# Optimization experiments

Hardware: AMD Instinct MI355X
Metric: run time of the kernel (lower is better)

## Reference

```python
import jax, jax.numpy as jnp
import numpy as np

N_EXPERTS, D_MODEL, D_FF, TOP_K, N_TOKENS = 8, 1024, 4096, 2, 8192

def _uniform_init(key, shape, fan_in):
    # matches torch init: gain = sqrt(1/3), std = gain/sqrt(fan_in), bound = sqrt(3)*std
    bound = np.sqrt(3.0) * np.sqrt(1.0 / 3.0) / np.sqrt(fan_in)
    return jax.random.uniform(key, shape, minval=-bound, maxval=bound, dtype=jnp.float32)

def setup_inputs() -> dict:
    key = jax.random.key(0)
    kx, ki, kw, k1, k2, k3 = jax.random.split(key, 6)
    x = jax.random.normal(kx, (N_TOKENS, D_MODEL), dtype=jnp.float32)
    expert_indices = jax.random.randint(ki, (N_TOKENS, TOP_K), 0, N_EXPERTS, dtype=jnp.int32)
    expert_weights = jax.random.uniform(kw, (N_TOKENS, TOP_K), dtype=jnp.float32)
    w1 = _uniform_init(k1, (N_EXPERTS, D_MODEL, D_FF), D_MODEL)
    w2 = _uniform_init(k2, (N_EXPERTS, D_MODEL, D_FF), D_MODEL)
    w3 = _uniform_init(k3, (N_EXPERTS, D_FF, D_MODEL), D_FF)
    return {"x": x, "expert_indices": expert_indices, "expert_weights": expert_weights,
            "w1": w1, "w2": w2, "w3": w3}

def reference(x, expert_indices, expert_weights, w1, w2, w3):
    # For each token t and routed expert e with routing weight p:
    #   out[t] += p * (silu(x[t] @ W1[e]) * (x[t] @ W2[e])) @ W3[e]
    # Loop over the small fixed expert set; compute each expert's SwiGLU FFN
    # densely over all tokens and combine with per-token routing weights
    # (mathematically identical to the sorted-dispatch grouped GEMM).
    n_experts = w1.shape[0]
    out = jnp.zeros_like(x)
    for e in range(n_experts):
        gate = x @ w1[e]                 # [N, d_ff]
        val = x @ w2[e]                  # [N, d_ff]
        y = (jax.nn.silu(gate) * val) @ w3[e]   # [N, d_model]
        # sum routing weights over top_k slots that picked expert e
        p = jnp.sum(jnp.where(expert_indices == e, expert_weights, 0.0), axis=1)
        out = out + p[:, None] * y
    return out
```

## Files before the change

kernel.cpp:

```cpp
#include <hip/hip_runtime.h>
#include <hip/hip_bf16.h>

typedef __attribute__((ext_vector_type(8))) short short8;
typedef __attribute__((ext_vector_type(4))) float f32x4;
typedef unsigned short u16;
typedef unsigned int u32;

#define NTOK   8192
#define DMODEL 1024
#define DFF    4096
#define NEXP   8
#define NPAIR  (NTOK * 2)
#define PADM   256
#define MT1    72
#define PPAD   (MT1 * PADM)
#define MT2    (PPAD / 128)

#define OFF_XB   0ull
#define OFF_W1T  (OFF_XB  + (size_t)NTOK * DMODEL * 2)
#define OFF_W2T  (OFF_W1T + (size_t)NEXP * DFF * DMODEL * 2)
#define OFF_W3T  (OFF_W2T + (size_t)NEXP * DFF * DMODEL * 2)
#define OFF_H    (OFF_W3T + (size_t)NEXP * DMODEL * DFF * 2)
#define OFF_TOK  (OFF_H   + (size_t)PPAD * DFF * 2)
#define OFF_WGT  (OFF_TOK + (size_t)PPAD * 4)
#define OFF_CNT  (OFF_WGT + (size_t)PPAD * 4)
#define OFF_CUR  (OFF_CNT + 64)
#define OFF_OFFP (OFF_CUR + 64)
#define WS_END   (OFF_OFFP + 64)

#define GLOAD16(gp, lp)                                                        \
  __builtin_amdgcn_global_load_lds(                                            \
      (const __attribute__((address_space(1))) u32*)(gp),                      \
      (__attribute__((address_space(3))) u32*)(lp), 16, 0, 0)

__device__ __forceinline__ u16 f2bu(float f) {
  __hip_bfloat16 b = __float2bfloat16(f);
  return __builtin_bit_cast(u16, b);
}


__global__ __launch_bounds__(256) void cvt_x_k(const float* __restrict__ x,
                                               u16* __restrict__ xb) {
  int i = blockIdx.x * 256 + threadIdx.x;
  float4 v = ((const float4*)x)[i];
  unsigned long long pk = (unsigned long long)f2bu(v.x) |
                          ((unsigned long long)f2bu(v.y) << 16) |
                          ((unsigned long long)f2bu(v.z) << 32) |
                          ((unsigned long long)f2bu(v.w) << 48);
  ((unsigned long long*)xb)[i] = pk;
}

__global__ __launch_bounds__(256) void tr_cvt_k(const float* __restrict__ src,
                                                u16* __restrict__ dst, int R, int C) {
  src += (size_t)blockIdx.z * R * C;
  dst += (size_t)blockIdx.z * R * C;
  int c0 = blockIdx.x * 64, r0 = blockIdx.y * 64;
  __shared__ float tile[64][65];
  int tid = threadIdx.x;
  int f4 = tid & 15, rr = tid >> 4;
#pragma unroll
  for (int p = 0; p < 4; ++p) {
    int r = rr + p * 16;
    float4 v = *(const float4*)(src + (size_t)(r0 + r) * C + c0 + f4 * 4);
    tile[r][f4 * 4 + 0] = v.x; tile[r][f4 * 4 + 1] = v.y;
    tile[r][f4 * 4 + 2] = v.z; tile[r][f4 * 4 + 3] = v.w;
  }
  __syncthreads();
  int ch = tid & 7, cc = tid >> 3;
#pragma unroll
  for (int p = 0; p < 2; ++p) {
    int c = cc + p * 32;
    short8 s;
#pragma unroll
    for (int j = 0; j < 8; ++j) s[j] = (short)f2bu(tile[ch * 8 + j][c]);
    *(short8*)(dst + (size_t)(c0 + c) * R + r0 + ch * 8) = s;
  }
}


__global__ __launch_bounds__(256) void count_k(const int* __restrict__ ei,
                                               int* __restrict__ cnt) {
  int i = blockIdx.x * 256 + threadIdx.x;
  atomicAdd(&cnt[ei[i]], 1);
}

__global__ void scan_k(const int* __restrict__ cnt, int* __restrict__ offp) {
  if (threadIdx.x == 0) {
    int a = 0;
#pragma unroll
    for (int e = 0; e < NEXP; ++e) { offp[e] = a; a += (cnt[e] + PADM - 1) & ~(PADM - 1); }
    offp[NEXP] = a;
  }
}

__global__ __launch_bounds__(256) void scatter_k(const int* __restrict__ ei,
                                                 const float* __restrict__ ew,
                                                 const int* __restrict__ offp,
                                                 int* __restrict__ cur,
                                                 int* __restrict__ tok,
                                                 float* __restrict__ wg) {
  int i = blockIdx.x * 256 + threadIdx.x;
  int e = ei[i];
  int p = offp[e] + atomicAdd(&cur[e], 1);
  tok[p] = i >> 1;
  wg[p] = ew[i];
}


#define S1_BUF 16384
#define S1_NK  32

__global__ __launch_bounds__(512, 2) void stage1_k(const u16* __restrict__ xb,
                                                   const u16* __restrict__ w1t,
                                                   const u16* __restrict__ w2t,
                                                   u16* __restrict__ h,
                                                   const int* __restrict__ tok,
                                                   const int* __restrict__ offp) {
  extern __shared__ __align__(16) u16 lds[];
  const int r0 = blockIdx.y * PADM;
  if (r0 >= offp[NEXP]) return;
  int e = 0;
#pragma unroll
  for (int q = 0; q < 7; ++q) e += (offp[e + 1] <= r0) ? 1 : 0;
  const int n0 = blockIdx.x * 128;
  const int tid = threadIdx.x;
  const int lane = tid & 63, w = tid >> 6;
  const int wm = w >> 2, wn = w & 3;

  const int sl = lane & 3, rl = lane >> 2;
  const u16* aga[2];
  int adb[2];
#pragma unroll
  for (int j = 0; j < 2; ++j) {
    int row = w * 32 + j * 16 + rl;
    int t = tok[r0 + row];
    aga[j] = xb + (size_t)t * DMODEL + ((sl ^ ((row >> 1) & 3)) << 3);
    adb[j] = (w * 32 + j * 16) * 32;
  }
  const u16* w1e = w1t + (size_t)e * DFF * DMODEL;
  const u16* w2e = w2t + (size_t)e * DFF * DMODEL;
  const u16* bg1; const u16* bg2;
  int bdb;
  {
    int row = w * 16 + rl;
    size_t ro = (size_t)(n0 + row) * DMODEL + ((sl ^ ((row >> 1) & 3)) << 3);
    bg1 = w1e + ro; bg2 = w2e + ro;
    bdb = (w * 16) * 32;
  }

  int aoff[8], boff[2];
  {
    int ks = lane >> 4;
#pragma unroll
    for (int mi = 0; mi < 8; ++mi) {
      int row = wm * 128 + mi * 16 + (lane & 15);
      aoff[mi] = row * 32 + ((ks ^ ((row >> 1) & 3)) << 3);
    }
#pragma unroll
    for (int ni = 0; ni < 2; ++ni) {
      int col = wn * 32 + ni * 16 + (lane & 15);
      boff[ni] = col * 32 + ((ks ^ ((col >> 1) & 3)) << 3);
    }
  }

  f32x4 accg[8][2], accv[8][2];
  const f32x4 zero = {0.f, 0.f, 0.f, 0.f};
#pragma unroll
  for (int mi = 0; mi < 8; ++mi)
#pragma unroll
    for (int ni = 0; ni < 2; ++ni) { accg[mi][ni] = zero; accv[mi][ni] = zero; }

#define S1_ISSUE(Q, KO)                                                        \
  do {                                                                         \
    GLOAD16(aga[0] + (KO), (Q) + adb[0]);                                      \
    GLOAD16(aga[1] + (KO), (Q) + adb[1]);                                      \
    GLOAD16(bg1 + (KO), (Q) + 8192 + bdb);                                     \
    GLOAD16(bg2 + (KO), (Q) + 12288 + bdb);                                    \
  } while (0)

  S1_ISSUE(lds, 0);
  S1_ISSUE(lds + S1_BUF, 32);
  asm volatile("s_waitcnt vmcnt(4)" ::: "memory");
  __builtin_amdgcn_s_barrier();
  __builtin_amdgcn_sched_barrier(0);

#define S1_STEP(P, KC, ISSUE)                                                  \
  {                                                                            \
    const u16* Ab  = lds + (P) * S1_BUF;                                       \
    const u16* B1b = Ab + 8192;                                                \
    const u16* B2b = Ab + 12288;                                               \
    short8 af[8], b1f[2], b2f[2];                                              \
    _Pragma("unroll") for (int mi = 0; mi < 8; ++mi)                           \
      af[mi] = *(const short8*)(Ab + aoff[mi]);                                \
    _Pragma("unroll") for (int ni = 0; ni < 2; ++ni) {                         \
      b1f[ni] = *(const short8*)(B1b + boff[ni]);                              \
      b2f[ni] = *(const short8*)(B2b + boff[ni]);                              \
    }                                                                          \
    if (ISSUE) S1_ISSUE(lds + (((P) + 2) % 3) * S1_BUF, ((KC) + 2) * 32);      \
    __builtin_amdgcn_s_setprio(1);                                             \
    _Pragma("unroll") for (int mi = 0; mi < 8; ++mi)                           \
      _Pragma("unroll") for (int ni = 0; ni < 2; ++ni) {                       \
        accg[mi][ni] = __builtin_amdgcn_mfma_f32_16x16x32_bf16(                \
            af[mi], b1f[ni], accg[mi][ni], 0, 0, 0);                           \
        accv[mi][ni] = __builtin_amdgcn_mfma_f32_16x16x32_bf16(                \
            af[mi], b2f[ni], accv[mi][ni], 0, 0, 0);                           \
      }                                                                        \
    __builtin_amdgcn_s_setprio(0);                                             \
    if (ISSUE) asm volatile("s_waitcnt vmcnt(4)" ::: "memory");                \
    else       asm volatile("s_waitcnt vmcnt(0)" ::: "memory");                \
    __builtin_amdgcn_s_barrier();                                              \
    __builtin_amdgcn_sched_barrier(0);                                         \
  }

  for (int kc = 0; kc < S1_NK - 2; kc += 3) {
    S1_STEP(0, kc, 1)
    S1_STEP(1, kc + 1, 1)
    S1_STEP(2, kc + 2, 1)
  }
  S1_STEP(0, S1_NK - 2, 0)
  S1_STEP(1, S1_NK - 1, 0)
#undef S1_STEP
#undef S1_ISSUE

  const int prow = r0 + wm * 128 + ((lane >> 4) << 2);
  const int pcol = n0 + wn * 32 + (lane & 15);
#pragma unroll
  for (int mi = 0; mi < 8; ++mi)
#pragma unroll
    for (int ni = 0; ni < 2; ++ni)
#pragma unroll
      for (int j = 0; j < 4; ++j) {
        float g = accg[mi][ni][j];
        float v = accv[mi][ni][j];
        float s = g / (1.f + __expf(-g));
        h[(size_t)(prow + mi * 16 + j) * DFF + (pcol + ni * 16)] = f2bu(s * v);
      }
}


__global__ __launch_bounds__(256) void stage2_k(const u16* __restrict__ h,
                                                const u16* __restrict__ w3t,
                                                float* __restrict__ out,
                                                const int* __restrict__ tok,
                                                const float* __restrict__ wg,
                                                const int* __restrict__ offp) {
  __shared__ __align__(16) u16 As[128 * 64];
  __shared__ __align__(16) u16 Bs[64 * 64];
  const int r0 = blockIdx.y * 128;
  if (r0 >= offp[NEXP]) return;
  int e = 0;
#pragma unroll
  for (int q = 0; q < 7; ++q) e += (offp[e + 1] <= r0) ? 1 : 0;
  const int n0 = blockIdx.x * 64;
  const int tid = threadIdx.x;
  const int lane = tid & 63, w = tid >> 6;
  const int wm = w >> 1, wn = w & 1;
  const int lr = lane >> 3, seg = lane & 7;

  const u16* aga[4];
#pragma unroll
  for (int j = 0; j < 4; ++j) {
    int rowl = w * 32 + j * 8 + lr;
    aga[j] = h + (size_t)(r0 + rowl) * DFF + ((seg ^ (rowl & 7)) << 3);
  }
  const u16* w3e = w3t + (size_t)e * DMODEL * DFF;
  const u16* bga[2];
#pragma unroll
  for (int j = 0; j < 2; ++j) {
    int coll = w * 16 + j * 8 + lr;
    bga[j] = w3e + (size_t)(n0 + coll) * DFF + ((seg ^ (coll & 7)) << 3);
  }
  u16 *Ad[4], *Bd[2];
#pragma unroll
  for (int j = 0; j < 4; ++j) Ad[j] = As + (w * 32 + j * 8) * 64;
#pragma unroll
  for (int j = 0; j < 2; ++j) Bd[j] = Bs + (w * 16 + j * 8) * 64;

  int aoff[4][2], boff[2][2];
  {
    int ar = wm * 64 + (lane & 15), ks = lane >> 4;
#pragma unroll
    for (int mi = 0; mi < 4; ++mi)
#pragma unroll
      for (int kk = 0; kk < 2; ++kk) {
        int row = ar + mi * 16;
        aoff[mi][kk] = row * 64 + (((kk * 4 + ks) ^ (row & 7)) << 3);
      }
    int bc = wn * 32 + (lane & 15);
#pragma unroll
    for (int ni = 0; ni < 2; ++ni)
#pragma unroll
      for (int kk = 0; kk < 2; ++kk) {
        int col = bc + ni * 16;
        boff[ni][kk] = col * 64 + (((kk * 4 + ks) ^ (col & 7)) << 3);
      }
  }

  f32x4 acc[4][2];
  const f32x4 zero = {0.f, 0.f, 0.f, 0.f};
#pragma unroll
  for (int mi = 0; mi < 4; ++mi)
#pragma unroll
    for (int ni = 0; ni < 2; ++ni) acc[mi][ni] = zero;

  for (int kc = 0; kc < DFF / 64; ++kc) {
    const int ko = kc * 64;
#pragma unroll
    for (int j = 0; j < 4; ++j) GLOAD16(aga[j] + ko, Ad[j]);
#pragma unroll
    for (int j = 0; j < 2; ++j) GLOAD16(bga[j] + ko, Bd[j]);
    __syncthreads();
#pragma unroll
    for (int kk = 0; kk < 2; ++kk) {
      short8 a[4], b[2];
#pragma unroll
      for (int mi = 0; mi < 4; ++mi) a[mi] = *(const short8*)(As + aoff[mi][kk]);
#pragma unroll
      for (int ni = 0; ni < 2; ++ni) b[ni] = *(const short8*)(Bs + boff[ni][kk]);
#pragma unroll
      for (int mi = 0; mi < 4; ++mi)
#pragma unroll
        for (int ni = 0; ni < 2; ++ni)
          acc[mi][ni] = __builtin_amdgcn_mfma_f32_16x16x32_bf16(a[mi], b[ni], acc[mi][ni], 0, 0, 0);
    }
    __syncthreads();
  }

  const int prow = r0 + wm * 64 + ((lane >> 4) << 2);
  const int pcol = n0 + wn * 32 + (lane & 15);
#pragma unroll
  for (int mi = 0; mi < 4; ++mi)
#pragma unroll
    for (int j = 0; j < 4; ++j) {
      int pos = prow + mi * 16 + j;
      float p = wg[pos];
      if (p != 0.f) {
        int t = tok[pos];
#pragma unroll
        for (int ni = 0; ni < 2; ++ni)
          atomicAdd(&out[(size_t)t * DMODEL + pcol + ni * 16], p * acc[mi][ni][j]);
      }
    }
}


extern "C" void kernel_launch(void* const* d_in, const int* in_sizes, int n_in,
                              void* d_out, int out_size, void* d_ws, size_t ws_size,
                              hipStream_t stream) {
  (void)in_sizes; (void)n_in;
  const float* x  = (const float*)d_in[0];
  const int*   ei = (const int*)d_in[1];
  const float* ew = (const float*)d_in[2];
  const float* w1 = (const float*)d_in[3];
  const float* w2 = (const float*)d_in[4];
  const float* w3 = (const float*)d_in[5];
  float* out = (float*)d_out;
  char* ws = (char*)d_ws;

  hipMemsetAsync(out, 0, (size_t)out_size * sizeof(float), stream);
  if (ws_size < WS_END) return;

  u16* xb   = (u16*)(ws + OFF_XB);
  u16* w1t  = (u16*)(ws + OFF_W1T);
  u16* w2t  = (u16*)(ws + OFF_W2T);
  u16* w3t  = (u16*)(ws + OFF_W3T);
  u16* hb   = (u16*)(ws + OFF_H);
  int* tok  = (int*)(ws + OFF_TOK);
  float* wg = (float*)(ws + OFF_WGT);
  int* cnt  = (int*)(ws + OFF_CNT);
  int* cur  = (int*)(ws + OFF_CUR);
  int* offp = (int*)(ws + OFF_OFFP);

  hipMemsetAsync(ws + OFF_TOK, 0, (size_t)(WS_END - OFF_TOK), stream);

  hipFuncSetAttribute(reinterpret_cast<const void*>(stage1_k),
                      hipFuncAttributeMaxDynamicSharedMemorySize, 98304);

  cvt_x_k<<<dim3(NTOK * DMODEL / 4 / 256), 256, 0, stream>>>(x, xb);
  tr_cvt_k<<<dim3(DFF / 64, DMODEL / 64, NEXP), 256, 0, stream>>>(w1, w1t, DMODEL, DFF);
  tr_cvt_k<<<dim3(DFF / 64, DMODEL / 64, NEXP), 256, 0, stream>>>(w2, w2t, DMODEL, DFF);
  tr_cvt_k<<<dim3(DMODEL / 64, DFF / 64, NEXP), 256, 0, stream>>>(w3, w3t, DFF, DMODEL);
  count_k<<<dim3(NPAIR / 256), 256, 0, stream>>>(ei, cnt);
  scan_k<<<1, 64, 0, stream>>>(cnt, offp);
  scatter_k<<<dim3(NPAIR / 256), 256, 0, stream>>>(ei, ew, offp, cur, tok, wg);
  stage1_k<<<dim3(DFF / 128, MT1), 512, 98304, stream>>>(xb, w1t, w2t, hb, tok, offp);
  stage2_k<<<dim3(DMODEL / 64, MT2), 256, 0, stream>>>(hb, w3t, out, tok, wg, offp);
}
```

Baseline: 842.5 us.

## Use 32x32 MFMA in stage1 and pipeline stage2 with larger tiles

Stage1 switches from 16x16x32 to 32x32x16 bf16 MFMA instructions, cutting the number of LDS fragment reads per MFMA and changing the epilogue row mapping. Stage2 is rewritten from a single-buffered 128x64 tile with 256 threads to a 256x128 tile with 512 threads and a triple-buffered global_load_lds pipeline in dynamic LDS, modelled on stage1. This aims to overlap W3/h loads with compute and raise data reuse in the down-projection. The cost is higher register and LDS use per block, fewer blocks, and more atomics per thread in the epilogue.

```diff
diff --git a/kernel.cpp b/kernel.cpp
--- a/kernel.cpp
+++ b/kernel.cpp
@@ -3,6 +3,7 @@
 
 typedef __attribute__((ext_vector_type(8))) short short8;
 typedef __attribute__((ext_vector_type(4))) float f32x4;
+typedef __attribute__((ext_vector_type(16))) float f32x16;
 typedef unsigned short u16;
 typedef unsigned int u32;
 
@@ -14,7 +15,6 @@
 #define PADM   256
 #define MT1    72
 #define PPAD   (MT1 * PADM)
-#define MT2    (PPAD / 128)
 
 #define OFF_XB   0ull
 #define OFF_W1T  (OFF_XB  + (size_t)NTOK * DMODEL * 2)
@@ -148,27 +148,24 @@
     bdb = (w * 16) * 32;
   }
 
-  int aoff[8], boff[2];
+  int aoff[4], boff;
   {
-    int ks = lane >> 4;
-#pragma unroll
-    for (int mi = 0; mi < 8; ++mi) {
-      int row = wm * 128 + mi * 16 + (lane & 15);
-      aoff[mi] = row * 32 + ((ks ^ ((row >> 1) & 3)) << 3);
+    int kg0 = lane >> 5;
+#pragma unroll
+    for (int mb = 0; mb < 4; ++mb) {
+      int row = wm * 128 + mb * 32 + (lane & 31);
+      aoff[mb] = row * 32 + ((kg0 ^ ((row >> 1) & 3)) << 3);
     }
-#pragma unroll
-    for (int ni = 0; ni < 2; ++ni) {
-      int col = wn * 32 + ni * 16 + (lane & 15);
-      boff[ni] = col * 32 + ((ks ^ ((col >> 1) & 3)) << 3);
-    }
-  }
-
-  f32x4 accg[8][2], accv[8][2];
-  const f32x4 zero = {0.f, 0.f, 0.f, 0.f};
-#pragma unroll
-  for (int mi = 0; mi < 8; ++mi)
-#pragma unroll
-    for (int ni = 0; ni < 2; ++ni) { accg[mi][ni] = zero; accv[mi][ni] = zero; }
+    int col = wn * 32 + (lane & 31);
+    boff = col * 32 + ((kg0 ^ ((col >> 1) & 3)) << 3);
+  }
+
+  f32x16 accg[4], accv[4];
+#pragma unroll
+  for (int mb = 0; mb < 4; ++mb) {
+#pragma unroll
+    for (int r = 0; r < 16; ++r) { accg[mb][r] = 0.f; accv[mb][r] = 0.f; }
+  }
 
 #define S1_ISSUE(Q, KO)                                                        \
   do {                                                                         \
@@ -189,21 +186,22 @@
     const u16* Ab  = lds + (P) * S1_BUF;                                       \
     const u16* B1b = Ab + 8192;                                                \
     const u16* B2b = Ab + 12288;                                               \
-    short8 af[8], b1f[2], b2f[2];                                              \
-    _Pragma("unroll") for (int mi = 0; mi < 8; ++mi)                           \
-      af[mi] = *(const short8*)(Ab + aoff[mi]);                                \
-    _Pragma("unroll") for (int ni = 0; ni < 2; ++ni) {                         \
-      b1f[ni] = *(const short8*)(B1b + boff[ni]);                              \
-      b2f[ni] = *(const short8*)(B2b + boff[ni]);                              \
+    short8 af[4][2], b1f[2], b2f[2];                                           \
+    _Pragma("unroll") for (int mb = 0; mb < 4; ++mb)                           \
+      _Pragma("unroll") for (int kk = 0; kk < 2; ++kk)                         \
+        af[mb][kk] = *(const short8*)(Ab + (aoff[mb] ^ (kk << 4)));            \
+    _Pragma("unroll") for (int kk = 0; kk < 2; ++kk) {                         \
+      b1f[kk] = *(const short8*)(B1b + (boff ^ (kk << 4)));                    \
+      b2f[kk] = *(const short8*)(B2b + (boff ^ (kk << 4)));                    \
     }                                                                          \
     if (ISSUE) S1_ISSUE(lds + (((P) + 2) % 3) * S1_BUF, ((KC) + 2) * 32);      \
     __builtin_amdgcn_s_setprio(1);                                             \
-    _Pragma("unroll") for (int mi = 0; mi < 8; ++mi)                           \
-      _Pragma("unroll") for (int ni = 0; ni < 2; ++ni) {                       \
-        accg[mi][ni] = __builtin_amdgcn_mfma_f32_16x16x32_bf16(                \
-            af[mi], b1f[ni], accg[mi][ni], 0, 0, 0);                           \
-        accv[mi][ni] = __builtin_amdgcn_mfma_f32_16x16x32_bf16(                \
-            af[mi], b2f[ni], accv[mi][ni], 0, 0, 0);                           \
+    _Pragma("unroll") for (int kk = 0; kk < 2; ++kk)                           \
+      _Pragma("unroll") for (int mb = 0; mb < 4; ++mb) {                       \
+        accg[mb] = __builtin_amdgcn_mfma_f32_32x32x16_bf16(                    \
+            af[mb][kk], b1f[kk], accg[mb], 0, 0, 0);                           \
+        accv[mb] = __builtin_amdgcn_mfma_f32_32x32x16_bf16(                    \
+            af[mb][kk], b2f[kk], accv[mb], 0, 0, 0);                           \
       }                                                                        \
     __builtin_amdgcn_s_setprio(0);                                             \
     if (ISSUE) asm volatile("s_waitcnt vmcnt(4)" ::: "memory");                \
@@ -222,112 +220,140 @@
 #undef S1_STEP
 #undef S1_ISSUE
 
-  const int prow = r0 + wm * 128 + ((lane >> 4) << 2);
-  const int pcol = n0 + wn * 32 + (lane & 15);
-#pragma unroll
-  for (int mi = 0; mi < 8; ++mi)
-#pragma unroll
-    for (int ni = 0; ni < 2; ++ni)
-#pragma unroll
-      for (int j = 0; j < 4; ++j) {
-        float g = accg[mi][ni][j];
-        float v = accv[mi][ni][j];
-        float s = g / (1.f + __expf(-g));
-        h[(size_t)(prow + mi * 16 + j) * DFF + (pcol + ni * 16)] = f2bu(s * v);
-      }
-}
-
-
-__global__ __launch_bounds__(256) void stage2_k(const u16* __restrict__ h,
-                                                const u16* __restrict__ w3t,
-                                                float* __restrict__ out,
-                                                const int* __restrict__ tok,
-                                                const float* __restrict__ wg,
-                                                const int* __restrict__ offp) {
-  __shared__ __align__(16) u16 As[128 * 64];
-  __shared__ __align__(16) u16 Bs[64 * 64];
-  const int r0 = blockIdx.y * 128;
+  const int ecol = n0 + wn * 32 + (lane & 31);
+  const int erow0 = r0 + wm * 128 + 4 * (lane >> 5);
+#pragma unroll
+  for (int mb = 0; mb < 4; ++mb)
+#pragma unroll
+    for (int r = 0; r < 16; ++r) {
+      int erow = erow0 + mb * 32 + (r & 3) + 8 * (r >> 2);
+      float g = accg[mb][r];
+      float v = accv[mb][r];
+      float s = g / (1.f + __expf(-g));
+      h[(size_t)erow * DFF + ecol] = f2bu(s * v);
+    }
+}
+
+
+#define S2_BUF 12288
+#define S2_NK  128
+
+__global__ __launch_bounds__(512, 4) void stage2_k(const u16* __restrict__ h,
+                                                   const u16* __restrict__ w3t,
+                                                   float* __restrict__ out,
+                                                   const int* __restrict__ tok,
+                                                   const float* __restrict__ wg,
+                                                   const int* __restrict__ offp) {
+  extern __shared__ __align__(16) u16 lds[];
+  const int r0 = blockIdx.y * 256;
   if (r0 >= offp[NEXP]) return;
   int e = 0;
 #pragma unroll
   for (int q = 0; q < 7; ++q) e += (offp[e + 1] <= r0) ? 1 : 0;
-  const int n0 = blockIdx.x * 64;
+  const int n0 = blockIdx.x * 128;
   const int tid = threadIdx.x;
   const int lane = tid & 63, w = tid >> 6;
   const int wm = w >> 1, wn = w & 1;
-  const int lr = lane >> 3, seg = lane & 7;
-
-  const u16* aga[4];
-#pragma unroll
-  for (int j = 0; j < 4; ++j) {
-    int rowl = w * 32 + j * 8 + lr;
-    aga[j] = h + (size_t)(r0 + rowl) * DFF + ((seg ^ (rowl & 7)) << 3);
+
+  const int sl = lane & 3, rl = lane >> 2;
+  const u16* aga[2];
+  int adb[2];
+#pragma unroll
+  for (int j = 0; j < 2; ++j) {
+    int row = w * 32 + j * 16 + rl;
+    aga[j] = h + (size_t)(r0 + row) * DFF + ((sl ^ ((row >> 1) & 3)) << 3);
+    adb[j] = (w * 32 + j * 16) * 32;
   }
   const u16* w3e = w3t + (size_t)e * DMODEL * DFF;
-  const u16* bga[2];
-#pragma unroll
-  for (int j = 0; j < 2; ++j) {
-    int coll = w * 16 + j * 8 + lr;
-    bga[j] = w3e + (size_t)(n0 + coll) * DFF + ((seg ^ (coll & 7)) << 3);
-  }
-  u16 *Ad[4], *Bd[2];
-#pragma unroll
-  for (int j = 0; j < 4; ++j) Ad[j] = As + (w * 32 + j * 8) * 64;
-#pragma unroll
-  for (int j = 0; j < 2; ++j) Bd[j] = Bs + (w * 16 + j * 8) * 64;
-
-  int aoff[4][2], boff[2][2];
+  const u16* bga;
+  int bdb;
   {
-    int ar = wm * 64 + (lane & 15), ks = lane >> 4;
-#pragma unroll
-    for (int mi = 0; mi < 4; ++mi)
-#pragma unroll
-      for (int kk = 0; kk < 2; ++kk) {
-        int row = ar + mi * 16;
-        aoff[mi][kk] = row * 64 + (((kk * 4 + ks) ^ (row & 7)) << 3);
-      }
-    int bc = wn * 32 + (lane & 15);
-#pragma unroll
-    for (int ni = 0; ni < 2; ++ni)
-#pragma unroll
-      for (int kk = 0; kk < 2; ++kk) {
-        int col = bc + ni * 16;
-        boff[ni][kk] = col * 64 + (((kk * 4 + ks) ^ (col & 7)) << 3);
-      }
-  }
-
-  f32x4 acc[4][2];
+    int row = w * 16 + rl;
+    bga = w3e + (size_t)(n0 + row) * DFF + ((sl ^ ((row >> 1) & 3)) << 3);
+    bdb = (w * 16) * 32;
+  }
+
+  int aoff[4], boff[4];
+  {
+    int ks = lane >> 4;
+#pragma unroll
+    for (int mi = 0; mi < 4; ++mi) {
+      int row = wm * 64 + mi * 16 + (lane & 15);
+      aoff[mi] = row * 32 + ((ks ^ ((row >> 1) & 3)) << 3);
+    }
+#pragma unroll
+    for (int ni = 0; ni < 4; ++ni) {
+      int col = wn * 64 + ni * 16 + (lane & 15);
+      boff[ni] = col * 32 + ((ks ^ ((col >> 1) & 3)) << 3);
+    }
+  }
+
+  f32x4 acc[4][4];
   const f32x4 zero = {0.f, 0.f, 0.f, 0.f};
 #pragma unroll
   for (int mi = 0; mi < 4; ++mi)
 #pragma unroll
-    for (int ni = 0; ni < 2; ++ni) acc[mi][ni] = zero;
-
-  for (int kc = 0; kc < DFF / 64; ++kc) {
-    const int ko = kc * 64;
-#pragma unroll
-    for (int j = 0; j < 4; ++j) GLOAD16(aga[j] + ko, Ad[j]);
-#pragma unroll
-    for (int j = 0; j < 2; ++j) GLOAD16(bga[j] + ko, Bd[j]);
-    __syncthreads();
-#pragma unroll
-    for (int kk = 0; kk < 2; ++kk) {
-      short8 a[4], b[2];
-#pragma unroll
-      for (int mi = 0; mi < 4; ++mi) a[mi] = *(const short8*)(As + aoff[mi][kk]);
-#pragma unroll
-      for (int ni = 0; ni < 2; ++ni) b[ni] = *(const short8*)(Bs + boff[ni][kk]);
-#pragma unroll
-      for (int mi = 0; mi < 4; ++mi)
-#pragma unroll
-        for (int ni = 0; ni < 2; ++ni)
-          acc[mi][ni] = __builtin_amdgcn_mfma_f32_16x16x32_bf16(a[mi], b[ni], acc[mi][ni], 0, 0, 0);
-    }
-    __syncthreads();
-  }
+    for (int ni = 0; ni < 4; ++ni) acc[mi][ni] = zero;
+
+#define S2_ISSUE(Q, KO)                                                        \
+  do {                                                                         \
+    GLOAD16(aga[0] + (KO), (Q) + adb[0]);                                      \
+    GLOAD16(aga[1] + (KO), (Q) + adb[1]);                                      \
+    GLOAD16(bga + (KO), (Q) + 8192 + bdb);                                     \
+  } while (0)
+
+  S2_ISSUE(lds, 0);
+  S2_ISSUE(lds + S2_BUF, 32);
+  asm volatile("s_waitcnt vmcnt(3)" ::: "memory");
+  __builtin_amdgcn_s_barrier();
+  __builtin_amdgcn_sched_barrier(0);
+
+#define S2_STEP(P, KC, ISSUE)                                                  \
+  {                                                                            \
+    const u16* Ab = lds + (P) * S2_BUF;                                        \
+    const u16* Bb = Ab + 8192;                                                 \
+    short8 bf[4], af0, af1;                                                    \
+    _Pragma("unroll") for (int ni = 0; ni < 4; ++ni)                           \
+      bf[ni] = *(const short8*)(Bb + boff[ni]);                                \
+    af0 = *(const short8*)(Ab + aoff[0]);                                      \
+    af1 = *(const short8*)(Ab + aoff[1]);                                      \
+    if (ISSUE) S2_ISSUE(lds + (((P) + 2) % 3) * S2_BUF, ((KC) + 2) * 32);      \
+    __builtin_amdgcn_s_setprio(1);                                             \
+    _Pragma("unroll") for (int ni = 0; ni < 4; ++ni) {                         \
+      acc[0][ni] = __builtin_amdgcn_mfma_f32_16x16x32_bf16(                    \
+          af0, bf[ni], acc[0][ni], 0, 0, 0);                                   \
+      acc[1][ni] = __builtin_amdgcn_mfma_f32_16x16x32_bf16(                    \
+          af1, bf[ni], acc[1][ni], 0, 0, 0);                                   \
+    }                                                                          \
+    __builtin_amdgcn_s_setprio(0);                                             \
+    af0 = *(const short8*)(Ab + aoff[2]);                                      \
+    af1 = *(const short8*)(Ab + aoff[3]);                                      \
+    __builtin_amdgcn_s_setprio(1);                                             \
+    _Pragma("unroll") for (int ni = 0; ni < 4; ++ni) {                         \
+      acc[2][ni] = __builtin_amdgcn_mfma_f32_16x16x32_bf16(                    \
+          af0, bf[ni], acc[2][ni], 0, 0, 0);                                   \
+      acc[3][ni] = __builtin_amdgcn_mfma_f32_16x16x32_bf16(                    \
+          af1, bf[ni], acc[3][ni], 0, 0, 0);                                   \
+    }                                                                          \
+    __builtin_amdgcn_s_setprio(0);                                             \
+    if (ISSUE) asm volatile("s_waitcnt vmcnt(3)" ::: "memory");                \
+    else       asm volatile("s_waitcnt vmcnt(0)" ::: "memory");                \
+    __builtin_amdgcn_s_barrier();                                              \
+    __builtin_amdgcn_sched_barrier(0);                                         \
+  }
+
+  for (int kc = 0; kc < S2_NK - 2; kc += 3) {
+    S2_STEP(0, kc, 1)
+    S2_STEP(1, kc + 1, 1)
+    S2_STEP(2, kc + 2, 1)
+  }
+  S2_STEP(0, S2_NK - 2, 0)
+  S2_STEP(1, S2_NK - 1, 0)
+#undef S2_STEP
+#undef S2_ISSUE
 
   const int prow = r0 + wm * 64 + ((lane >> 4) << 2);
-  const int pcol = n0 + wn * 32 + (lane & 15);
+  const int pcolb = n0 + wn * 64 + (lane & 15);
 #pragma unroll
   for (int mi = 0; mi < 4; ++mi)
 #pragma unroll
@@ -337,8 +363,8 @@
       if (p != 0.f) {
         int t = tok[pos];
 #pragma unroll
-        for (int ni = 0; ni < 2; ++ni)
-          atomicAdd(&out[(size_t)t * DMODEL + pcol + ni * 16], p * acc[mi][ni][j]);
+        for (int ni = 0; ni < 4; ++ni)
+          atomicAdd(&out[(size_t)t * DMODEL + pcolb + ni * 16], p * acc[mi][ni][j]);
       }
     }
 }
@@ -375,6 +401,8 @@
 
   hipFuncSetAttribute(reinterpret_cast<const void*>(stage1_k),
                       hipFuncAttributeMaxDynamicSharedMemorySize, 98304);
+  hipFuncSetAttribute(reinterpret_cast<const void*>(stage2_k),
+                      hipFuncAttributeMaxDynamicSharedMemorySize, 73728);
 
   cvt_x_k<<<dim3(NTOK * DMODEL / 4 / 256), 256, 0, stream>>>(x, xb);
   tr_cvt_k<<<dim3(DFF / 64, DMODEL / 64, NEXP), 256, 0, stream>>>(w1, w1t, DMODEL, DFF);
@@ -384,5 +412,5 @@
   scan_k<<<1, 64, 0, stream>>>(cnt, offp);
   scatter_k<<<dim3(NPAIR / 256), 256, 0, stream>>>(ei, ew, offp, cur, tok, wg);
   stage1_k<<<dim3(DFF / 128, MT1), 512, 98304, stream>>>(xb, w1t, w2t, hb, tok, offp);
-  stage2_k<<<dim3(DMODEL / 64, MT2), 256, 0, stream>>>(hb, w3t, out, tok, wg, offp);
-}
+  stage2_k<<<dim3(DMODEL / 128, PPAD / 256), 512, 73728, stream>>>(hb, w3t, out, tok, wg, offp);
+}
```

Result: slower. 862.8 us (+2.4%).

## Enlarge stage2 tiles and triple-buffer LDS loads with async pipelining

Applied to the files above, without the earlier changes.

Rewrites the down-projection grouped GEMM to use 256x128 tiles with 512 threads, so each wave computes a 64x64 sub-tile. The single-buffered load/sync/compute loop becomes a three-stage pipeline of direct global-to-LDS loads. Explicit vmcnt waits and raw barriers let loads for step k+2 overlap MFMA work on step k, and setprio raises priority during the MFMA bursts. The goal is better operand reuse and hidden memory latency. The cost is 144KB of dynamic LDS per block, which limits occupancy to one block per CU, and fewer blocks in the grid.

```diff
diff --git a/kernel.cpp b/kernel.cpp
--- a/kernel.cpp
+++ b/kernel.cpp
@@ -14,7 +14,6 @@
 #define PADM   256
 #define MT1    72
 #define PPAD   (MT1 * PADM)
-#define MT2    (PPAD / 128)
 
 #define OFF_XB   0ull
 #define OFF_W1T  (OFF_XB  + (size_t)NTOK * DMODEL * 2)
@@ -238,96 +237,126 @@
 }
 
 
-__global__ __launch_bounds__(256) void stage2_k(const u16* __restrict__ h,
-                                                const u16* __restrict__ w3t,
-                                                float* __restrict__ out,
-                                                const int* __restrict__ tok,
-                                                const float* __restrict__ wg,
-                                                const int* __restrict__ offp) {
-  __shared__ __align__(16) u16 As[128 * 64];
-  __shared__ __align__(16) u16 Bs[64 * 64];
-  const int r0 = blockIdx.y * 128;
+#define S2_BUF 24576
+#define S2_NK  64
+
+__global__ __launch_bounds__(512, 2) void stage2_k(const u16* __restrict__ h,
+                                                   const u16* __restrict__ w3t,
+                                                   float* __restrict__ out,
+                                                   const int* __restrict__ tok,
+                                                   const float* __restrict__ wg,
+                                                   const int* __restrict__ offp) {
+  extern __shared__ __align__(16) u16 lds[];
+  const int r0 = blockIdx.y * 256;
   if (r0 >= offp[NEXP]) return;
   int e = 0;
 #pragma unroll
   for (int q = 0; q < 7; ++q) e += (offp[e + 1] <= r0) ? 1 : 0;
-  const int n0 = blockIdx.x * 64;
+  const int n0 = blockIdx.x * 128;
   const int tid = threadIdx.x;
   const int lane = tid & 63, w = tid >> 6;
   const int wm = w >> 1, wn = w & 1;
   const int lr = lane >> 3, seg = lane & 7;
 
   const u16* aga[4];
+  int adb[4];
 #pragma unroll
   for (int j = 0; j < 4; ++j) {
-    int rowl = w * 32 + j * 8 + lr;
-    aga[j] = h + (size_t)(r0 + rowl) * DFF + ((seg ^ (rowl & 7)) << 3);
+    int row = w * 32 + j * 8 + lr;
+    aga[j] = h + (size_t)(r0 + row) * DFF + ((seg ^ (row & 7)) << 3);
+    adb[j] = (w * 32 + j * 8) * 64;
   }
   const u16* w3e = w3t + (size_t)e * DMODEL * DFF;
   const u16* bga[2];
+  int bdb[2];
 #pragma unroll
   for (int j = 0; j < 2; ++j) {
-    int coll = w * 16 + j * 8 + lr;
-    bga[j] = w3e + (size_t)(n0 + coll) * DFF + ((seg ^ (coll & 7)) << 3);
-  }
-  u16 *Ad[4], *Bd[2];
-#pragma unroll
-  for (int j = 0; j < 4; ++j) Ad[j] = As + (w * 32 + j * 8) * 64;
-#pragma unroll
-  for (int j = 0; j < 2; ++j) Bd[j] = Bs + (w * 16 + j * 8) * 64;
-
-  int aoff[4][2], boff[2][2];
+    int row = w * 16 + j * 8 + lr;
+    bga[j] = w3e + (size_t)(n0 + row) * DFF + ((seg ^ (row & 7)) << 3);
+    bdb[j] = (w * 16 + j * 8) * 64;
+  }
+
+  int aoff[4][2], boff[4][2];
   {
-    int ar = wm * 64 + (lane & 15), ks = lane >> 4;
+    int ks = lane >> 4;
 #pragma unroll
     for (int mi = 0; mi < 4; ++mi)
 #pragma unroll
       for (int kk = 0; kk < 2; ++kk) {
-        int row = ar + mi * 16;
+        int row = wm * 64 + mi * 16 + (lane & 15);
         aoff[mi][kk] = row * 64 + (((kk * 4 + ks) ^ (row & 7)) << 3);
       }
-    int bc = wn * 32 + (lane & 15);
-#pragma unroll
-    for (int ni = 0; ni < 2; ++ni)
+#pragma unroll
+    for (int ni = 0; ni < 4; ++ni)
 #pragma unroll
       for (int kk = 0; kk < 2; ++kk) {
-        int col = bc + ni * 16;
+        int col = wn * 64 + ni * 16 + (lane & 15);
         boff[ni][kk] = col * 64 + (((kk * 4 + ks) ^ (col & 7)) << 3);
       }
   }
 
-  f32x4 acc[4][2];
+  f32x4 acc[4][4];
   const f32x4 zero = {0.f, 0.f, 0.f, 0.f};
 #pragma unroll
   for (int mi = 0; mi < 4; ++mi)
 #pragma unroll
-    for (int ni = 0; ni < 2; ++ni) acc[mi][ni] = zero;
-
-  for (int kc = 0; kc < DFF / 64; ++kc) {
-    const int ko = kc * 64;
-#pragma unroll
-    for (int j = 0; j < 4; ++j) GLOAD16(aga[j] + ko, Ad[j]);
-#pragma unroll
-    for (int j = 0; j < 2; ++j) GLOAD16(bga[j] + ko, Bd[j]);
-    __syncthreads();
-#pragma unroll
-    for (int kk = 0; kk < 2; ++kk) {
-      short8 a[4], b[2];
-#pragma unroll
-      for (int mi = 0; mi < 4; ++mi) a[mi] = *(const short8*)(As + aoff[mi][kk]);
-#pragma unroll
-      for (int ni = 0; ni < 2; ++ni) b[ni] = *(const short8*)(Bs + boff[ni][kk]);
-#pragma unroll
-      for (int mi = 0; mi < 4; ++mi)
-#pragma unroll
-        for (int ni = 0; ni < 2; ++ni)
-          acc[mi][ni] = __builtin_amdgcn_mfma_f32_16x16x32_bf16(a[mi], b[ni], acc[mi][ni], 0, 0, 0);
-    }
-    __syncthreads();
-  }
+    for (int ni = 0; ni < 4; ++ni) acc[mi][ni] = zero;
+
+#define S2_ISSUE(Q, KO)                                                        \
+  do {                                                                         \
+    GLOAD16(aga[0] + (KO), (Q) + adb[0]);                                      \
+    GLOAD16(aga[1] + (KO), (Q) + adb[1]);                                      \
+    GLOAD16(aga[2] + (KO), (Q) + adb[2]);                                      \
+    GLOAD16(aga[3] + (KO), (Q) + adb[3]);                                      \
+    GLOAD16(bga[0] + (KO), (Q) + 16384 + bdb[0]);                              \
+    GLOAD16(bga[1] + (KO), (Q) + 16384 + bdb[1]);                              \
+  } while (0)
+
+  S2_ISSUE(lds, 0);
+  S2_ISSUE(lds + S2_BUF, 64);
+  asm volatile("s_waitcnt vmcnt(6)" ::: "memory");
+  __builtin_amdgcn_s_barrier();
+  __builtin_amdgcn_sched_barrier(0);
+
+#define S2_STEP(P, KC, ISSUE)                                                  \
+  {                                                                            \
+    const u16* Ab = lds + (P) * S2_BUF;                                        \
+    const u16* Bb = Ab + 16384;                                                \
+    short8 af[4][2], bf[4][2];                                                 \
+    _Pragma("unroll") for (int mi = 0; mi < 4; ++mi)                           \
+      _Pragma("unroll") for (int kk = 0; kk < 2; ++kk)                         \
+        af[mi][kk] = *(const short8*)(Ab + aoff[mi][kk]);                      \
+    _Pragma("unroll") for (int ni = 0; ni < 4; ++ni)                           \
+      _Pragma("unroll") for (int kk = 0; kk < 2; ++kk)                         \
+        bf[ni][kk] = *(const short8*)(Bb + boff[ni][kk]);                      \
+    if (ISSUE) S2_ISSUE(lds + (((P) + 2) % 3) * S2_BUF, ((KC) + 2) * 64);      \
+    __builtin_amdgcn_s_setprio(1);                                             \
+    _Pragma("unroll") for (int kk = 0; kk < 2; ++kk)                           \
+      _Pragma("unroll") for (int mi = 0; mi < 4; ++mi)                         \
+        _Pragma("unroll") for (int ni = 0; ni < 4; ++ni)                       \
+          acc[mi][ni] = __builtin_amdgcn_mfma_f32_16x16x32_bf16(               \
+              af[mi][kk], bf[ni][kk], acc[mi][ni], 0, 0, 0);                   \
+    __builtin_amdgcn_s_setprio(0);                                             \
+    if (ISSUE) asm volatile("s_waitcnt vmcnt(6)" ::: "memory");                \
+    else       asm volatile("s_waitcnt vmcnt(0)" ::: "memory");                \
+    __builtin_amdgcn_s_barrier();                                              \
+    __builtin_amdgcn_sched_barrier(0);                                         \
+  }
+
+  for (int kc = 0; kc < S2_NK - 4; kc += 3) {
+    S2_STEP(0, kc, 1)
+    S2_STEP(1, kc + 1, 1)
+    S2_STEP(2, kc + 2, 1)
+  }
+  S2_STEP(0, S2_NK - 4, 1)
+  S2_STEP(1, S2_NK - 3, 1)
+  S2_STEP(2, S2_NK - 2, 0)
+  S2_STEP(0, S2_NK - 1, 0)
+#undef S2_STEP
+#undef S2_ISSUE
 
   const int prow = r0 + wm * 64 + ((lane >> 4) << 2);
-  const int pcol = n0 + wn * 32 + (lane & 15);
+  const int pcolb = n0 + wn * 64 + (lane & 15);
 #pragma unroll
   for (int mi = 0; mi < 4; ++mi)
 #pragma unroll
@@ -337,8 +366,8 @@
       if (p != 0.f) {
         int t = tok[pos];
 #pragma unroll
-        for (int ni = 0; ni < 2; ++ni)
-          atomicAdd(&out[(size_t)t * DMODEL + pcol + ni * 16], p * acc[mi][ni][j]);
+        for (int ni = 0; ni < 4; ++ni)
+          atomicAdd(&out[(size_t)t * DMODEL + pcolb + ni * 16], p * acc[mi][ni][j]);
       }
     }
 }
@@ -375,6 +404,8 @@
 
   hipFuncSetAttribute(reinterpret_cast<const void*>(stage1_k),
                       hipFuncAttributeMaxDynamicSharedMemorySize, 98304);
+  hipFuncSetAttribute(reinterpret_cast<const void*>(stage2_k),
+                      hipFuncAttributeMaxDynamicSharedMemorySize, 147456);
 
   cvt_x_k<<<dim3(NTOK * DMODEL / 4 / 256), 256, 0, stream>>>(x, xb);
   tr_cvt_k<<<dim3(DFF / 64, DMODEL / 64, NEXP), 256, 0, stream>>>(w1, w1t, DMODEL, DFF);
@@ -384,5 +415,5 @@
   scan_k<<<1, 64, 0, stream>>>(cnt, offp);
   scatter_k<<<dim3(NPAIR / 256), 256, 0, stream>>>(ei, ew, offp, cur, tok, wg);
   stage1_k<<<dim3(DFF / 128, MT1), 512, 98304, stream>>>(xb, w1t, w2t, hb, tok, offp);
-  stage2_k<<<dim3(DMODEL / 64, MT2), 256, 0, stream>>>(hb, w3t, out, tok, wg, offp);
-}
+  stage2_k<<<dim3(DMODEL / 128, PPAD / 256), 512, 147456, stream>>>(hb, w3t, out, tok, wg, offp);
+}
```

New measurement: 820.3 us. 1.03x faster.
